# Kernel optimization log

Hardware: AMD Instinct MI355X
Metric: run time of the kernel (lower is better)

## Reference

```python
import jax, jax.numpy as jnp
import numpy as np

H, KV, D, HID = 16, 4, 64, 1024
OUT_MIN, OUT_MAX = 32, 8192  # output_size_max = config.max_position_embeddings


def _score_attn(x, Wq, Wk, Wv, Wo):
    # Full (non-causal, unmasked) GQA attention whose o_proj maps to 1 scalar/token.
    B, S, _ = x.shape
    q = (x @ Wq).reshape(B, S, H, D)
    k = jnp.repeat((x @ Wk).reshape(B, S, KV, D), H // KV, axis=2)  # repeat_kv
    v = jnp.repeat((x @ Wv).reshape(B, S, KV, D), H // KV, axis=2)
    scores = jnp.einsum('bqhd,bkhd->bhqk', q, k) / jnp.asarray(np.sqrt(D), x.dtype)
    a = jax.nn.softmax(scores, axis=-1)
    o = jnp.einsum('bhqk,bkhd->bqhd', a, v).reshape(B, S, H * D)
    return o @ Wo  # (B, S, 1)


def _dynamic_sizes(x, Wq, Wk, Wv, Wo, scale):
    s = _score_attn(x, Wq, Wk, Wv, Wo)               # (B,S,1)
    means = jax.nn.sigmoid(s).mean(axis=1)            # (B,1) (no attention_mask)
    sizes = means.squeeze(-1) * scale * (OUT_MAX - OUT_MIN) + OUT_MIN
    return sizes.astype(jnp.int32)                    # torch .int() truncation


def _segment_ids(sizes_np, S, max_len):
    # torch.linspace(0, L, sz+1).long() boundaries; token t -> segment i with
    # intervals[i] <= t < intervals[i+1]; right-aligned into [max_len] per batch.
    B = len(sizes_np)
    seg = np.zeros((B, S), np.int32)
    t = np.arange(S)
    for b, sz in enumerate(sizes_np):
        sz = int(sz)
        bnd = np.floor(np.linspace(0.0, S, sz + 1, dtype=np.float64)).astype(np.int64)
        s = np.clip(np.searchsorted(bnd, t, side='right') - 1, 0, sz - 1)
        seg[b] = b * max_len + (max_len - sz) + s
    return jnp.asarray(seg)


def setup_inputs() -> dict:
    key = jax.random.key(0)
    ks = jax.random.split(key, 10)
    B, S = 4, 2048
    x = jax.random.normal(ks[0], (B, S, HID), jnp.float32)
    def lin(k, i, o):
        return jax.random.normal(k, (i, o), jnp.float32) / np.sqrt(i).astype(np.float32)
    return dict(
        hidden_states=x,
        Wq1=lin(ks[1], HID, H * D), Wk1=lin(ks[2], HID, KV * D),
        Wv1=lin(ks[3], HID, KV * D), Wo1=lin(ks[4], H * D, 1),
        Wq2=lin(ks[5], HID, H * D), Wk2=lin(ks[6], HID, KV * D),
        Wv2=lin(ks[7], HID, KV * D), Wo2=lin(ks[8], H * D, 1),
        scale_param=jnp.asarray(0.01, jnp.float32),
    )


def reference(hidden_states, Wq1, Wk1, Wv1, Wo1, Wq2, Wk2, Wv2, Wo2, scale_param):
    B, S, Hd = hidden_states.shape
    # 1) size-estimation attention -> per-batch dynamic output sizes (data-dependent shape)
    sizes = _dynamic_sizes(hidden_states, Wq1, Wk1, Wv1, Wo1, scale_param)
    sizes_np = np.asarray(jax.device_get(sizes))
    max_len = int(sizes_np.max())
    seg = _segment_ids(sizes_np, S, max_len)          # (B,S) global segment ids
    # 2) weighted-pooling attention -> per-token sigmoid weights
    w = jax.nn.sigmoid(_score_attn(hidden_states, Wq2, Wk2, Wv2, Wo2)).squeeze(-1)  # (B,S)
    # 3) weighted average pooling over dynamic-size segments (vectorized scatter-add)
    num = jax.ops.segment_sum((hidden_states * w[..., None]).reshape(B * S, Hd),
                              seg.reshape(-1), num_segments=B * max_len)
    den = jax.ops.segment_sum(w.reshape(-1), seg.reshape(-1), num_segments=B * max_len)
    pooled = (num / (den[:, None] + 1e-8)).reshape(B, max_len, Hd)
    out_mask = jnp.arange(max_len)[None, :] >= (max_len - sizes)[:, None]
    return pooled, out_mask, sizes
```

## Files before the change

kernel.cpp:

```cpp
#include <hip/hip_runtime.h>
#include <math.h>

#define TB 256

constexpr int B_ = 4, S_ = 2048, HID_ = 1024, H_ = 16, KV_ = 4, D_ = 64;

typedef short sh8 __attribute__((ext_vector_type(8)));
typedef float fl4 __attribute__((ext_vector_type(4)));
typedef unsigned short u16;
typedef unsigned int u32;

__device__ __forceinline__ u16 f2bf(float f) {
  u32 u = __float_as_uint(f);
  u += 0x7fff + ((u >> 16) & 1);
  return (u16)(u >> 16);
}
__device__ __forceinline__ float bf2f(u16 h) { return __uint_as_float(((u32)h) << 16); }

constexpr size_t XSZ   = (size_t)B_ * S_ * HID_;
constexpr size_t WQH_O = 2 * XSZ;
constexpr size_t WQSZ  = (size_t)2 * HID_ * (H_ * D_);
constexpr size_t WQL_O = WQH_O + WQSZ;
constexpr size_t WKH_O = WQH_O + 2 * WQSZ;
constexpr size_t WKSZ  = (size_t)2 * HID_ * (KV_ * D_);
constexpr size_t WKL_O = WKH_O + WKSZ;
constexpr size_t KH_O  = WKH_O + 2 * WKSZ;
constexpr size_t KSZ   = (size_t)2 * B_ * KV_ * S_ * D_;
constexpr size_t KL_O  = KH_O + KSZ;
constexpr size_t KPLANE = (size_t)S_ * D_;
constexpr size_t FBASE   = (KH_O + 2 * KSZ) / 2;
constexpr size_t U_OFF   = FBASE;
constexpr size_t U_SZ    = (size_t)2 * B_ * H_ * S_;
constexpr size_t WVO_OFF = U_OFF + U_SZ;
constexpr size_t WVO_SZ  = (size_t)HID_ * 32;
constexpr size_t SH_OFF  = WVO_OFF + WVO_SZ;
constexpr size_t SH_SZ   = (size_t)2 * B_ * S_ * H_;
constexpr size_t W_OFF   = SH_OFF + SH_SZ;
constexpr size_t W_SZ    = (size_t)B_ * S_;
constexpr size_t SUM_OFF = W_OFF + W_SZ;

__device__ __forceinline__ void conv_w_body(
    const float* __restrict__ W1, const float* __restrict__ W2,
    u16* __restrict__ OH, u16* __restrict__ OL, int ncols,
    int blk, int tid, float wt[32][257]) {
  int ngrp = ncols >> 8;
  int a = blk / (32 * ngrp);
  int rem = blk - a * 32 * ngrp;
  int cs = rem / ngrp, ng = rem - cs * ngrp;
  const float* W = a ? W2 : W1;
#pragma unroll
  for (int i = 0; i < 8; ++i) {
    int e = tid + i * 256;
    int r = e >> 6, c4 = (e & 63) * 4;
    float4 v = *reinterpret_cast<const float4*>(
        W + ((size_t)(cs * 32 + r)) * ncols + ng * 256 + c4);
    wt[r][c4] = v.x; wt[r][c4 + 1] = v.y; wt[r][c4 + 2] = v.z; wt[r][c4 + 3] = v.w;
  }
  __syncthreads();
  int w = tid >> 6, lane = tid & 63, quad = lane >> 4, col = lane & 15;
  int NF = ncols >> 4;
#pragma unroll
  for (int f = 0; f < 4; ++f) {
    int n16 = w * 4 + f;
    sh8 hh, ll;
#pragma unroll
    for (int j = 0; j < 8; ++j) {
      float v = wt[quad * 8 + j][n16 * 16 + col];
      u16 hb = f2bf(v);
      hh[j] = (short)hb;
      ll[j] = (short)f2bf(v - bf2f(hb));
    }
    size_t fb = (((size_t)a * 32 + cs) * NF + ng * 16 + n16) * 512 + (size_t)lane * 8;
    *reinterpret_cast<sh8*>(OH + fb) = hh;
    *reinterpret_cast<sh8*>(OL + fb) = ll;
  }
}

__global__ __launch_bounds__(TB) void prep1_kernel(
    const float* __restrict__ x,
    const float* __restrict__ Wq1, const float* __restrict__ Wq2,
    const float* __restrict__ Wk1, const float* __restrict__ Wk2,
    const float* __restrict__ Wv1, const float* __restrict__ Wo1,
    const float* __restrict__ Wv2, const float* __restrict__ Wo2,
    float* __restrict__ ws) {
  __shared__ float wt[32][257];
  int blk = blockIdx.x, tid = threadIdx.x;
  u16* wsu = (u16*)ws;
  if (blk < 512) {
    u16* XH = wsu;
    u16* XL = XH + XSZ;
    int bt = blk;
    int w = tid >> 6, lane = tid & 63, quad = lane >> 4, col = lane & 15;
    int b = bt >> 7, t16 = bt & 127;
    const float* row = x + ((size_t)b * S_ + t16 * 16 + col) * HID_;
#pragma unroll
    for (int i = 0; i < 8; ++i) {
      int cs = w + i * 4;
      const float* src = row + cs * 32 + quad * 8;
      float4 v0 = *reinterpret_cast<const float4*>(src);
      float4 v1 = *reinterpret_cast<const float4*>(src + 4);
      float vv[8] = {v0.x, v0.y, v0.z, v0.w, v1.x, v1.y, v1.z, v1.w};
      sh8 hh, ll;
#pragma unroll
      for (int j = 0; j < 8; ++j) {
        u16 hb = f2bf(vv[j]);
        hh[j] = (short)hb;
        ll[j] = (short)f2bf(vv[j] - bf2f(hb));
      }
      size_t fb = ((size_t)bt * 32 + cs) * 512 + (size_t)lane * 8;
      *reinterpret_cast<sh8*>(XH + fb) = hh;
      *reinterpret_cast<sh8*>(XL + fb) = ll;
    }
  } else if (blk < 768) {
    conv_w_body(Wq1, Wq2, wsu + WQH_O, wsu + WQL_O, H_ * D_, blk - 512, tid, wt);
  } else if (blk < 832) {
    conv_w_body(Wk1, Wk2, wsu + WKH_O, wsu + WKL_O, KV_ * D_, blk - 768, tid, wt);
  } else {
    int n = blk - 832, a = n >> 4, h = n & 15, kv = h >> 2;
    if (n == 0 && tid < 8) ws[SUM_OFF + tid] = 0.f;
    const float* Wv = a ? Wv2 : Wv1;
    const float* Wo = a ? Wo2 : Wo1;
    for (int c = tid; c < HID_; c += TB) {
      const float* vr = Wv + (size_t)c * (KV_ * D_) + kv * D_;
      const float* wo = Wo + h * D_;
      float acc = 0.f;
#pragma unroll 16
      for (int d = 0; d < D_; ++d) acc += vr[d] * wo[d];
      ws[WVO_OFF + (size_t)c * 32 + n] = acc;
    }
  }
}

__global__ __launch_bounds__(TB) void prep2_kernel(
    const float* __restrict__ x, float* __restrict__ ws) {
  __shared__ __align__(16) float xs[64][68];
  __shared__ float uw[64][36];
  int blk = blockIdx.x, tid = threadIdx.x;
  if (blk < 1024) {
    int k0 = (blk & 31) * 64;
    int kv = (blk >> 5) & 3;
    int ab = blk >> 7, a = ab >> 2, b = ab & 3;
    int w = tid >> 6, lane = tid & 63, quad = lane >> 4, col = lane & 15;
    const u16* XH = (const u16*)ws;
    const u16* XL = XH + XSZ;
    const u16* WKH = XH + WKH_O;
    const u16* WKL = XH + WKL_O;
    int tq = (w & 1) * 2, nq = (w >> 1) * 2;
    fl4 C[2][2] = {};
#pragma unroll 2
    for (int cs = 0; cs < 32; ++cs) {
      sh8 ah[2], al[2], bh[2], bl[2];
#pragma unroll
      for (int ti = 0; ti < 2; ++ti) {
        size_t fb = (((size_t)b * 128 + (k0 >> 4) + tq + ti) * 32 + cs) * 512 + (size_t)lane * 8;
        ah[ti] = *reinterpret_cast<const sh8*>(XH + fb);
        if (a == 0) al[ti] = *reinterpret_cast<const sh8*>(XL + fb);
      }
#pragma unroll
      for (int ni = 0; ni < 2; ++ni) {
        size_t fb = (((size_t)a * 32 + cs) * 16 + kv * 4 + nq + ni) * 512 + (size_t)lane * 8;
        bh[ni] = *reinterpret_cast<const sh8*>(WKH + fb);
        if (a == 0) bl[ni] = *reinterpret_cast<const sh8*>(WKL + fb);
      }
#pragma unroll
      for (int ti = 0; ti < 2; ++ti)
#pragma unroll
        for (int ni = 0; ni < 2; ++ni) {
          C[ti][ni] = __builtin_amdgcn_mfma_f32_16x16x32_bf16(ah[ti], bh[ni], C[ti][ni], 0, 0, 0);
          if (a == 0) {
            C[ti][ni] = __builtin_amdgcn_mfma_f32_16x16x32_bf16(al[ti], bh[ni], C[ti][ni], 0, 0, 0);
            C[ti][ni] = __builtin_amdgcn_mfma_f32_16x16x32_bf16(ah[ti], bl[ni], C[ti][ni], 0, 0, 0);
          }
        }
    }
#pragma unroll
    for (int ti = 0; ti < 2; ++ti)
#pragma unroll
      for (int ni = 0; ni < 2; ++ni)
#pragma unroll
        for (int r = 0; r < 4; ++r)
          xs[(tq + ti) * 16 + quad * 4 + r][(nq + ni) * 16 + col] = C[ti][ni][r];
    __syncthreads();
    u16* KH = (u16*)ws + KH_O;
    u16* KL = (u16*)ws + KL_O;
    size_t plane = (size_t)((a * B_ + b) * KV_ + kv) * KPLANE;
#pragma unroll
    for (int t = 0; t < 2; ++t) {
      int f = w + t * 4;
      int k16 = f & 3, ds = f >> 2;
      const float* row = &xs[k16 * 16 + col][ds * 32 + quad * 8];
      sh8 hh, ll;
#pragma unroll
      for (int j = 0; j < 8; ++j) {
        float v = row[j];
        u16 hb = f2bf(v);
        hh[j] = (short)hb;
        ll[j] = (short)f2bf(v - bf2f(hb));
      }
      size_t fb = plane + ((size_t)(((k0 >> 4) + k16) * 2 + ds)) * 512 + (size_t)lane * 8;
      *reinterpret_cast<sh8*>(KH + fb) = hh;
      if (a == 0) *reinterpret_cast<sh8*>(KL + fb) = ll;
    }
  } else {
    int i = blk - 1024;
    int k0 = (i & 31) * 64, b = i >> 5;
    int tk = tid >> 2, ng = tid & 3;
    int lr = tid >> 4, lc4 = (tid & 15) * 4;
    float acc[8] = {};
    for (int c0 = 0; c0 < HID_; c0 += 64) {
      __syncthreads();
#pragma unroll
      for (int p = 0; p < 4; ++p) {
        int r = lr + p * 16;
        *reinterpret_cast<float4*>(&xs[r][lc4]) =
            *reinterpret_cast<const float4*>(x + ((size_t)(b * S_ + k0 + r) * HID_ + c0 + lc4));
      }
      {
        int cc = tid >> 3, n4 = (tid & 7) * 4;
        *reinterpret_cast<float4*>(&uw[cc][n4]) =
            *reinterpret_cast<const float4*>(ws + WVO_OFF + (size_t)(c0 + cc) * 32 + n4);
        *reinterpret_cast<float4*>(&uw[cc + 32][n4]) =
            *reinterpret_cast<const float4*>(ws + WVO_OFF + (size_t)(c0 + cc + 32) * 32 + n4);
      }
      __syncthreads();
#pragma unroll 8
      for (int cc = 0; cc < 64; ++cc) {
        float xv = xs[tk][cc];
        float4 a0 = *reinterpret_cast<const float4*>(&uw[cc][ng * 8]);
        float4 a1 = *reinterpret_cast<const float4*>(&uw[cc][ng * 8 + 4]);
        acc[0] += xv * a0.x; acc[1] += xv * a0.y; acc[2] += xv * a0.z; acc[3] += xv * a0.w;
        acc[4] += xv * a1.x; acc[5] += xv * a1.y; acc[6] += xv * a1.z; acc[7] += xv * a1.w;
      }
    }
#pragma unroll
    for (int j = 0; j < 8; ++j) {
      int n = ng * 8 + j, a = n >> 4, h = n & 15;
      ws[U_OFF + ((size_t)(a * B_ + b) * H_ + h) * S_ + k0 + tk] = acc[j];
    }
  }
}

__global__ __launch_bounds__(TB, 4) void attn_kernel(float* __restrict__ ws) {
  __shared__ __align__(16) char smem[64 * 68 * 4];
  float (*Qt)[68] = reinterpret_cast<float(*)[68]>(smem);
  u16* kbuf = reinterpret_cast<u16*>(smem);
  int q0 = blockIdx.x * 64;
  int ah = blockIdx.y, a = ah >> 3, hp = ah & 7;
  int h0 = hp * 2, kv = hp >> 1;
  int b = blockIdx.z;
  int tid = threadIdx.x, w = tid >> 6, lane = tid & 63, quad = lane >> 4, col = lane & 15;
  const u16* XH = (const u16*)ws;
  const u16* XL = XH + XSZ;
  const u16* WQH = XH + WQH_O;
  const u16* WQL = XH + WQL_O;

  sh8 qh[2][2], ql[2][2];
#pragma unroll
  for (int e = 0; e < 2; ++e) {
    int h = h0 + e;
    int tq = (w & 1) * 2, nq = (w >> 1) * 2;
    fl4 C[2][2] = {};
#pragma unroll 2
    for (int cs = 0; cs < 32; ++cs) {
      sh8 ah_[2], al_[2], bh_[2], bl_[2];
#pragma unroll
      for (int ti = 0; ti < 2; ++ti) {
        size_t fb = (((size_t)b * 128 + (q0 >> 4) + tq + ti) * 32 + cs) * 512 + (size_t)lane * 8;
        ah_[ti] = *reinterpret_cast<const sh8*>(XH + fb);
        if (a == 0) al_[ti] = *reinterpret_cast<const sh8*>(XL + fb);
      }
#pragma unroll
      for (int ni = 0; ni < 2; ++ni) {
        size_t fb = (((size_t)a * 32 + cs) * 64 + h * 4 + nq + ni) * 512 + (size_t)lane * 8;
        bh_[ni] = *reinterpret_cast<const sh8*>(WQH + fb);
        if (a == 0) bl_[ni] = *reinterpret_cast<const sh8*>(WQL + fb);
      }
#pragma unroll
      for (int ti = 0; ti < 2; ++ti)
#pragma unroll
        for (int ni = 0; ni < 2; ++ni) {
          C[ti][ni] = __builtin_amdgcn_mfma_f32_16x16x32_bf16(ah_[ti], bh_[ni], C[ti][ni], 0, 0, 0);
          if (a == 0) {
            C[ti][ni] = __builtin_amdgcn_mfma_f32_16x16x32_bf16(al_[ti], bh_[ni], C[ti][ni], 0, 0, 0);
            C[ti][ni] = __builtin_amdgcn_mfma_f32_16x16x32_bf16(ah_[ti], bl_[ni], C[ti][ni], 0, 0, 0);
          }
        }
    }
    __syncthreads();
#pragma unroll
    for (int ti = 0; ti < 2; ++ti)
#pragma unroll
      for (int ni = 0; ni < 2; ++ni)
#pragma unroll
        for (int r = 0; r < 4; ++r)
          Qt[(nq + ni) * 16 + col][(tq + ti) * 16 + quad * 4 + r] = C[ti][ni][r];
    __syncthreads();
#pragma unroll
    for (int ds = 0; ds < 2; ++ds)
#pragma unroll
      for (int j = 0; j < 8; ++j) {
        float v = Qt[ds * 32 + quad * 8 + j][w * 16 + col];
        u16 hb = f2bf(v);
        qh[e][ds][j] = (short)hb;
        if (a == 0) ql[e][ds][j] = (short)f2bf(v - bf2f(hb));
      }
  }

  const u16* KHg = (const u16*)ws + KH_O + (size_t)((a * B_ + b) * KV_ + kv) * KPLANE;
  const u16* KLg = (const u16*)ws + KL_O + (size_t)((a * B_ + b) * KV_ + kv) * KPLANE;
  int nld = (a == 0) ? 4 : 2;
  const u16* srcp[4];
#pragma unroll
  for (int i = 0; i < 4; ++i) {
    if (i < nld) {
      int c = tid + TB * i, f = c >> 6, ln = c & 63;
      if (a == 0) {
        int st = f >> 2, ds = (f >> 1) & 1, p = f & 1;
        srcp[i] = (p ? KLg : KHg) + ((size_t)(st * 2 + ds)) * 512 + (size_t)ln * 8;
      } else {
        int st = f >> 1, ds = f & 1;
        srcp[i] = KHg + ((size_t)(st * 2 + ds)) * 512 + (size_t)ln * 8;
      }
    }
  }
  const float* up0 = ws + U_OFF + ((size_t)(a * B_ + b) * H_ + h0) * S_ + col;
  const float* up1 = up0 + S_;
  float num[2][4] = {}, den[2][4] = {};
  for (int kt = 0; kt < 32; ++kt) {
    __syncthreads();
#pragma unroll
    for (int i = 0; i < 4; ++i)
      if (i < nld) {
        *reinterpret_cast<uint4*>(kbuf + (size_t)(tid + TB * i) * 8) =
            *reinterpret_cast<const uint4*>(srcp[i]);
        srcp[i] += 4096;
      }
    __syncthreads();
    float uv[2][4];
#pragma unroll
    for (int st = 0; st < 4; ++st) { uv[0][st] = up0[st * 16]; uv[1][st] = up1[st * 16]; }
    up0 += 64; up1 += 64;
    const sh8* kb = (const sh8*)kbuf;
#pragma unroll
    for (int st = 0; st < 4; ++st) {
      sh8 bh0, bh1, bl0, bl1;
      if (a == 0) {
        bh0 = kb[(st * 4 + 0) * 64 + lane];
        bl0 = kb[(st * 4 + 1) * 64 + lane];
        bh1 = kb[(st * 4 + 2) * 64 + lane];
        bl1 = kb[(st * 4 + 3) * 64 + lane];
      } else {
        bh0 = kb[(st * 2 + 0) * 64 + lane];
        bh1 = kb[(st * 2 + 1) * 64 + lane];
      }
#pragma unroll
      for (int e = 0; e < 2; ++e) {
        fl4 C = {0.f, 0.f, 0.f, 0.f};
        C = __builtin_amdgcn_mfma_f32_16x16x32_bf16(qh[e][0], bh0, C, 0, 0, 0);
        C = __builtin_amdgcn_mfma_f32_16x16x32_bf16(qh[e][1], bh1, C, 0, 0, 0);
        if (a == 0) {
          C = __builtin_amdgcn_mfma_f32_16x16x32_bf16(ql[e][0], bh0, C, 0, 0, 0);
          C = __builtin_amdgcn_mfma_f32_16x16x32_bf16(ql[e][1], bh1, C, 0, 0, 0);
          C = __builtin_amdgcn_mfma_f32_16x16x32_bf16(qh[e][0], bl0, C, 0, 0, 0);
          C = __builtin_amdgcn_mfma_f32_16x16x32_bf16(qh[e][1], bl1, C, 0, 0, 0);
        }
#pragma unroll
        for (int r = 0; r < 4; ++r) {
          float ex = __expf(C[r] * 0.125f);
          den[e][r] += ex;
          num[e][r] += ex * uv[e][st];
        }
      }
    }
  }
#pragma unroll
  for (int off = 1; off < 16; off <<= 1)
#pragma unroll
    for (int e = 0; e < 2; ++e)
#pragma unroll
      for (int r = 0; r < 4; ++r) {
        den[e][r] += __shfl_xor(den[e][r], off);
        num[e][r] += __shfl_xor(num[e][r], off);
      }
  if (col == 0) {
#pragma unroll
    for (int e = 0; e < 2; ++e)
#pragma unroll
      for (int r = 0; r < 4; ++r) {
        int q = q0 + w * 16 + quad * 4 + r;
        ws[SH_OFF + ((size_t)(a * B_ + b) * S_ + q) * H_ + h0 + e] = num[e][r] / den[e][r];
      }
  }
}

__global__ __launch_bounds__(TB) void post_kernel(float* __restrict__ ws) {
  int g = blockIdx.x * TB + threadIdx.x;
  int b = g >> 11, q = g & (S_ - 1);
  const float* sh = ws + SH_OFF;
  float s1 = 0.f, s2 = 0.f;
#pragma unroll
  for (int h = 0; h < H_; ++h) {
    s1 += sh[((size_t)b * S_ + q) * H_ + h];
    s2 += sh[((size_t)(B_ + b) * S_ + q) * H_ + h];
  }
  ws[W_OFF + g] = 1.f / (1.f + expf(-s2));
  double sig = 1.0 / (1.0 + exp(-(double)s1));
#pragma unroll
  for (int off = 1; off < 64; off <<= 1) sig += __shfl_xor(sig, off);
  __shared__ double red[4];
  int tid = threadIdx.x;
  if ((tid & 63) == 0) red[tid >> 6] = sig;
  __syncthreads();
  if (tid == 0)
    atomicAdd(reinterpret_cast<double*>(ws + SUM_OFF) + b,
              red[0] + red[1] + red[2] + red[3]);
}

__global__ __launch_bounds__(TB) void pool_kernel(
    const float* __restrict__ x, const float* __restrict__ scale_p,
    const float* __restrict__ ws, float* __restrict__ out, int max_len) {
  int p = blockIdx.x, b = blockIdx.y;
  double m = reinterpret_cast<const double*>(ws + SUM_OFF)[b] / (double)S_;
  double v = m * (double)(*scale_p) * (double)(8192 - 32) + 32.0;
  int sz = (int)v;
  int s = p - (max_len - sz);
  int tid = threadIdx.x;
  size_t obase = ((size_t)b * max_len + p) * HID_;
  size_t maskbase = (size_t)B_ * max_len * HID_;
  size_t sizebase = maskbase + (size_t)B_ * max_len;
  if (p == 0 && tid == 0) out[sizebase + b] = (float)sz;
  if (s < 0) {
    *reinterpret_cast<float4*>(out + obase + tid * 4) = make_float4(0.f, 0.f, 0.f, 0.f);
    if (tid == 0) out[maskbase + (size_t)b * max_len + p] = 0.f;
    return;
  }
  double step = (double)S_ / (double)sz;
  int t0 = (int)floor((double)s * step);
  int t1 = (s + 1 == sz) ? S_ : (int)floor((double)(s + 1) * step);
  const float* wv = ws + W_OFF + (size_t)b * S_;
  const float* xb = x + (size_t)b * S_ * HID_;
  float den = 0.f, acc0 = 0.f, acc1 = 0.f, acc2 = 0.f, acc3 = 0.f;
  for (int t = t0; t < t1; ++t) {
    float wt = wv[t];
    den += wt;
    float4 xv = *reinterpret_cast<const float4*>(xb + (size_t)t * HID_ + tid * 4);
    acc0 += xv.x * wt; acc1 += xv.y * wt; acc2 += xv.z * wt; acc3 += xv.w * wt;
  }
  float d = den + 1e-8f;
  *reinterpret_cast<float4*>(out + obase + tid * 4) =
      make_float4(acc0 / d, acc1 / d, acc2 / d, acc3 / d);
  if (tid == 0) out[maskbase + (size_t)b * max_len + p] = 1.f;
}

extern "C" void kernel_launch(void* const* d_in, const int* in_sizes, int n_in,
                              void* d_out, int out_size, void* d_ws, size_t ws_size,
                              hipStream_t stream) {
  const float* x    = (const float*)d_in[0];
  const float* Wq1  = (const float*)d_in[1];
  const float* Wk1  = (const float*)d_in[2];
  const float* Wv1  = (const float*)d_in[3];
  const float* Wo1  = (const float*)d_in[4];
  const float* Wq2  = (const float*)d_in[5];
  const float* Wk2  = (const float*)d_in[6];
  const float* Wv2  = (const float*)d_in[7];
  const float* Wo2  = (const float*)d_in[8];
  const float* scale = (const float*)d_in[9];
  float* ws  = (float*)d_ws;
  float* out = (float*)d_out;

  int max_len = (out_size - B_) / (B_ * (HID_ + 1));

  prep1_kernel<<<864, TB, 0, stream>>>(x, Wq1, Wq2, Wk1, Wk2, Wv1, Wo1, Wv2, Wo2, ws);
  prep2_kernel<<<1152, TB, 0, stream>>>(x, ws);
  attn_kernel<<<dim3(S_ / 64, 16, B_), TB, 0, stream>>>(ws);
  post_kernel<<<(B_ * S_) / TB, TB, 0, stream>>>(ws);
  pool_kernel<<<dim3(max_len, B_), TB, 0, stream>>>(x, scale, ws, out, max_len);
}
```

Baseline: 455.3 us.

## Template attention on pass type, process four heads per block in second pass, fold scale into exp2

The attention kernel body becomes a template on the pass index and heads-per-block. The first (high/low precision) pass keeps two heads per block, while the second (bf16-only) pass now handles all four heads of a KV group per block, so each K tile loaded into shared memory is reused across twice as many heads. Q is prescaled by log2(e)/sqrt(D) so the softmax uses a raw exp2 instruction instead of a multiply plus __expf. Compile-time branching removes runtime checks on the pass index. The grid shrinks from 16 to 12 head-groups, and the 4-head variant uses more registers, which may hurt occupancy.

```diff
diff --git a/kernel.cpp b/kernel.cpp
--- a/kernel.cpp
+++ b/kernel.cpp
@@ -39,6 +39,8 @@
 constexpr size_t W_SZ    = (size_t)B_ * S_;
 constexpr size_t SUM_OFF = W_OFF + W_SZ;
 
+#define QSCALE 0.18033688011112044f
+
 __device__ __forceinline__ void conv_w_body(
     const float* __restrict__ W1, const float* __restrict__ W2,
     u16* __restrict__ OH, u16* __restrict__ OL, int ncols,
@@ -240,23 +242,20 @@
   }
 }
 
-__global__ __launch_bounds__(TB, 4) void attn_kernel(float* __restrict__ ws) {
-  __shared__ __align__(16) char smem[64 * 68 * 4];
+template <int A, int NH>
+__device__ __forceinline__ void attn_body(
+    float* __restrict__ ws, char* smem, int q0, int kv, int h0, int b, int tid) {
   float (*Qt)[68] = reinterpret_cast<float(*)[68]>(smem);
   u16* kbuf = reinterpret_cast<u16*>(smem);
-  int q0 = blockIdx.x * 64;
-  int ah = blockIdx.y, a = ah >> 3, hp = ah & 7;
-  int h0 = hp * 2, kv = hp >> 1;
-  int b = blockIdx.z;
-  int tid = threadIdx.x, w = tid >> 6, lane = tid & 63, quad = lane >> 4, col = lane & 15;
+  int w = tid >> 6, lane = tid & 63, quad = lane >> 4, col = lane & 15;
   const u16* XH = (const u16*)ws;
   const u16* XL = XH + XSZ;
   const u16* WQH = XH + WQH_O;
   const u16* WQL = XH + WQL_O;
 
-  sh8 qh[2][2], ql[2][2];
-#pragma unroll
-  for (int e = 0; e < 2; ++e) {
+  sh8 qh[NH][2], ql[NH][2];
+#pragma unroll
+  for (int e = 0; e < NH; ++e) {
     int h = h0 + e;
     int tq = (w & 1) * 2, nq = (w >> 1) * 2;
     fl4 C[2][2] = {};
@@ -267,20 +266,20 @@
       for (int ti = 0; ti < 2; ++ti) {
         size_t fb = (((size_t)b * 128 + (q0 >> 4) + tq + ti) * 32 + cs) * 512 + (size_t)lane * 8;
         ah_[ti] = *reinterpret_cast<const sh8*>(XH + fb);
-        if (a == 0) al_[ti] = *reinterpret_cast<const sh8*>(XL + fb);
+        if (A == 0) al_[ti] = *reinterpret_cast<const sh8*>(XL + fb);
       }
 #pragma unroll
       for (int ni = 0; ni < 2; ++ni) {
-        size_t fb = (((size_t)a * 32 + cs) * 64 + h * 4 + nq + ni) * 512 + (size_t)lane * 8;
+        size_t fb = (((size_t)A * 32 + cs) * 64 + h * 4 + nq + ni) * 512 + (size_t)lane * 8;
         bh_[ni] = *reinterpret_cast<const sh8*>(WQH + fb);
-        if (a == 0) bl_[ni] = *reinterpret_cast<const sh8*>(WQL + fb);
+        if (A == 0) bl_[ni] = *reinterpret_cast<const sh8*>(WQL + fb);
       }
 #pragma unroll
       for (int ti = 0; ti < 2; ++ti)
 #pragma unroll
         for (int ni = 0; ni < 2; ++ni) {
           C[ti][ni] = __builtin_amdgcn_mfma_f32_16x16x32_bf16(ah_[ti], bh_[ni], C[ti][ni], 0, 0, 0);
-          if (a == 0) {
+          if (A == 0) {
             C[ti][ni] = __builtin_amdgcn_mfma_f32_16x16x32_bf16(al_[ti], bh_[ni], C[ti][ni], 0, 0, 0);
             C[ti][ni] = __builtin_amdgcn_mfma_f32_16x16x32_bf16(ah_[ti], bl_[ni], C[ti][ni], 0, 0, 0);
           }
@@ -299,52 +298,54 @@
     for (int ds = 0; ds < 2; ++ds)
 #pragma unroll
       for (int j = 0; j < 8; ++j) {
-        float v = Qt[ds * 32 + quad * 8 + j][w * 16 + col];
+        float v = Qt[ds * 32 + quad * 8 + j][w * 16 + col] * QSCALE;
         u16 hb = f2bf(v);
         qh[e][ds][j] = (short)hb;
-        if (a == 0) ql[e][ds][j] = (short)f2bf(v - bf2f(hb));
-      }
-  }
-
-  const u16* KHg = (const u16*)ws + KH_O + (size_t)((a * B_ + b) * KV_ + kv) * KPLANE;
-  const u16* KLg = (const u16*)ws + KL_O + (size_t)((a * B_ + b) * KV_ + kv) * KPLANE;
-  int nld = (a == 0) ? 4 : 2;
-  const u16* srcp[4];
-#pragma unroll
-  for (int i = 0; i < 4; ++i) {
-    if (i < nld) {
-      int c = tid + TB * i, f = c >> 6, ln = c & 63;
-      if (a == 0) {
-        int st = f >> 2, ds = (f >> 1) & 1, p = f & 1;
-        srcp[i] = (p ? KLg : KHg) + ((size_t)(st * 2 + ds)) * 512 + (size_t)ln * 8;
-      } else {
-        int st = f >> 1, ds = f & 1;
-        srcp[i] = KHg + ((size_t)(st * 2 + ds)) * 512 + (size_t)ln * 8;
-      }
-    }
-  }
-  const float* up0 = ws + U_OFF + ((size_t)(a * B_ + b) * H_ + h0) * S_ + col;
-  const float* up1 = up0 + S_;
-  float num[2][4] = {}, den[2][4] = {};
+        if (A == 0) ql[e][ds][j] = (short)f2bf(v - bf2f(hb));
+      }
+  }
+
+  const u16* KHg = (const u16*)ws + KH_O + (size_t)((A * B_ + b) * KV_ + kv) * KPLANE;
+  const u16* KLg = (const u16*)ws + KL_O + (size_t)((A * B_ + b) * KV_ + kv) * KPLANE;
+  constexpr int nld = (A == 0) ? 4 : 2;
+  const u16* srcp[nld];
+#pragma unroll
+  for (int i = 0; i < nld; ++i) {
+    int c = tid + TB * i, f = c >> 6, ln = c & 63;
+    if (A == 0) {
+      int st = f >> 2, ds = (f >> 1) & 1, p = f & 1;
+      srcp[i] = (p ? KLg : KHg) + ((size_t)(st * 2 + ds)) * 512 + (size_t)ln * 8;
+    } else {
+      int st = f >> 1, ds = f & 1;
+      srcp[i] = KHg + ((size_t)(st * 2 + ds)) * 512 + (size_t)ln * 8;
+    }
+  }
+  const float* up[NH];
+#pragma unroll
+  for (int e = 0; e < NH; ++e)
+    up[e] = ws + U_OFF + ((size_t)(A * B_ + b) * H_ + h0 + e) * S_ + col;
+  float num[NH][4] = {}, den[NH][4] = {};
   for (int kt = 0; kt < 32; ++kt) {
     __syncthreads();
 #pragma unroll
-    for (int i = 0; i < 4; ++i)
-      if (i < nld) {
-        *reinterpret_cast<uint4*>(kbuf + (size_t)(tid + TB * i) * 8) =
-            *reinterpret_cast<const uint4*>(srcp[i]);
-        srcp[i] += 4096;
-      }
+    for (int i = 0; i < nld; ++i) {
+      *reinterpret_cast<uint4*>(kbuf + (size_t)(tid + TB * i) * 8) =
+          *reinterpret_cast<const uint4*>(srcp[i]);
+      srcp[i] += 4096;
+    }
     __syncthreads();
-    float uv[2][4];
-#pragma unroll
-    for (int st = 0; st < 4; ++st) { uv[0][st] = up0[st * 16]; uv[1][st] = up1[st * 16]; }
-    up0 += 64; up1 += 64;
+    float uv[NH][4];
+#pragma unroll
+    for (int e = 0; e < NH; ++e) {
+#pragma unroll
+      for (int st = 0; st < 4; ++st) uv[e][st] = up[e][st * 16];
+      up[e] += 64;
+    }
     const sh8* kb = (const sh8*)kbuf;
 #pragma unroll
     for (int st = 0; st < 4; ++st) {
       sh8 bh0, bh1, bl0, bl1;
-      if (a == 0) {
+      if (A == 0) {
         bh0 = kb[(st * 4 + 0) * 64 + lane];
         bl0 = kb[(st * 4 + 1) * 64 + lane];
         bh1 = kb[(st * 4 + 2) * 64 + lane];
@@ -354,11 +355,11 @@
         bh1 = kb[(st * 2 + 1) * 64 + lane];
       }
 #pragma unroll
-      for (int e = 0; e < 2; ++e) {
+      for (int e = 0; e < NH; ++e) {
         fl4 C = {0.f, 0.f, 0.f, 0.f};
         C = __builtin_amdgcn_mfma_f32_16x16x32_bf16(qh[e][0], bh0, C, 0, 0, 0);
         C = __builtin_amdgcn_mfma_f32_16x16x32_bf16(qh[e][1], bh1, C, 0, 0, 0);
-        if (a == 0) {
+        if (A == 0) {
           C = __builtin_amdgcn_mfma_f32_16x16x32_bf16(ql[e][0], bh0, C, 0, 0, 0);
           C = __builtin_amdgcn_mfma_f32_16x16x32_bf16(ql[e][1], bh1, C, 0, 0, 0);
           C = __builtin_amdgcn_mfma_f32_16x16x32_bf16(qh[e][0], bl0, C, 0, 0, 0);
@@ -366,7 +367,7 @@
         }
 #pragma unroll
         for (int r = 0; r < 4; ++r) {
-          float ex = __expf(C[r] * 0.125f);
+          float ex = __builtin_amdgcn_exp2f(C[r]);
           den[e][r] += ex;
           num[e][r] += ex * uv[e][st];
         }
@@ -376,7 +377,7 @@
 #pragma unroll
   for (int off = 1; off < 16; off <<= 1)
 #pragma unroll
-    for (int e = 0; e < 2; ++e)
+    for (int e = 0; e < NH; ++e)
 #pragma unroll
       for (int r = 0; r < 4; ++r) {
         den[e][r] += __shfl_xor(den[e][r], off);
@@ -384,12 +385,26 @@
       }
   if (col == 0) {
 #pragma unroll
-    for (int e = 0; e < 2; ++e)
+    for (int e = 0; e < NH; ++e)
 #pragma unroll
       for (int r = 0; r < 4; ++r) {
         int q = q0 + w * 16 + quad * 4 + r;
-        ws[SH_OFF + ((size_t)(a * B_ + b) * S_ + q) * H_ + h0 + e] = num[e][r] / den[e][r];
-      }
+        ws[SH_OFF + ((size_t)(A * B_ + b) * S_ + q) * H_ + h0 + e] = num[e][r] / den[e][r];
+      }
+  }
+}
+
+__global__ __launch_bounds__(TB, 4) void attn_kernel(float* __restrict__ ws) {
+  __shared__ __align__(16) char smem[64 * 68 * 4];
+  int q0 = blockIdx.x * 64;
+  int ah = blockIdx.y;
+  int b = blockIdx.z;
+  int tid = threadIdx.x;
+  if (ah < 8) {
+    attn_body<0, 2>(ws, smem, q0, ah >> 1, ah * 2, b, tid);
+  } else {
+    int kv = ah - 8;
+    attn_body<1, 4>(ws, smem, q0, kv, kv * 4, b, tid);
   }
 }
 
@@ -472,7 +487,7 @@
 
   prep1_kernel<<<864, TB, 0, stream>>>(x, Wq1, Wq2, Wk1, Wk2, Wv1, Wo1, Wv2, Wo2, ws);
   prep2_kernel<<<1152, TB, 0, stream>>>(x, ws);
-  attn_kernel<<<dim3(S_ / 64, 16, B_), TB, 0, stream>>>(ws);
+  attn_kernel<<<dim3(S_ / 64, 12, B_), TB, 0, stream>>>(ws);
   post_kernel<<<(B_ * S_) / TB, TB, 0, stream>>>(ws);
   pool_kernel<<<dim3(max_len, B_), TB, 0, stream>>>(x, scale, ws, out, max_len);
 }
```

Result: slower. 548.7 us (+20.5%).
